# Optimization experiments

Hardware: AMD Instinct MI355X
Metric: run time of the kernel (lower is better)

The kernel has to match this reference:

```python
import jax, jax.numpy as jnp
import numpy as np

Q = 5
PAD = Q // 2
MAX_OFFSET = 5.0


def _conv3(x, w, b):
    # 3x3 SAME conv, NCHW / OIHW
    y = jax.lax.conv_general_dilated(x, w, (1, 1), 'SAME',
                                     dimension_numbers=('NCHW', 'OIHW', 'NCHW'))
    return y + b[None, :, None, None]


def _l2norm_c(x):
    # F.normalize(p=2, dim=1) with eps=1e-12
    n = jnp.sqrt(jnp.sum(x * x, axis=1, keepdims=True))
    return x / jnp.maximum(n, 1e-12)


def _cost_volume(Ha, Hb):
    # cost[b,k,h,w] = sum_c Ha[b,c,h,w] * Hb_pad[b,c,h+dy,w+dx], k = dy*Q+dx
    B, C, H, W = Ha.shape
    Ha = _l2norm_c(Ha)
    Hb = _l2norm_c(Hb)
    Hbp = jnp.pad(Hb, ((0, 0), (0, 0), (PAD, PAD), (PAD, PAD)))
    costs = [jnp.sum(Ha * jax.lax.dynamic_slice(Hbp, (0, 0, dy, dx), (B, C, H, W)), axis=1)
             for dy in range(Q) for dx in range(Q)]
    return jnp.stack(costs, axis=1)  # (B, Q*Q, H, W)


def _grid_sample_border(img, x, y):
    # bilinear, padding_mode='border', align_corners=True; x,y in pixel coords (B,H,W)
    B, C, H, W = img.shape
    x = jnp.clip(x, 0.0, W - 1.0)
    y = jnp.clip(y, 0.0, H - 1.0)
    x0 = jnp.floor(x)
    y0 = jnp.floor(y)
    x1 = jnp.minimum(x0 + 1.0, W - 1.0)
    y1 = jnp.minimum(y0 + 1.0, H - 1.0)
    wx = (x - x0)[:, None, :, :]
    wy = (y - y0)[:, None, :, :]
    x0i, x1i = x0.astype(jnp.int32), x1.astype(jnp.int32)
    y0i, y1i = y0.astype(jnp.int32), y1.astype(jnp.int32)
    imf = img.reshape(B, C, H * W)

    def gather(yi, xi):
        idx = (yi * W + xi).reshape(B, 1, H * W)
        return jnp.take_along_axis(imf, idx, axis=2).reshape(B, C, H, W)

    v00 = gather(y0i, x0i)
    v01 = gather(y0i, x1i)
    v10 = gather(y1i, x0i)
    v11 = gather(y1i, x1i)
    return (v00 * (1 - wx) * (1 - wy) + v01 * wx * (1 - wy)
            + v10 * (1 - wx) * wy + v11 * wx * wy)


def reference(pts_bev, img_bev, heatmap_pts, heatmap_img,
              fw1, fb1, fw2, fb2, gw1, gb1, gw2, gb2):
    B, C, H, W = pts_bev.shape
    dt = pts_bev.dtype
    # permute (0,1,3,2), detach, sigmoid
    hp = jax.nn.sigmoid(jax.lax.stop_gradient(jnp.transpose(heatmap_pts, (0, 1, 3, 2))))
    hi = jax.nn.sigmoid(jax.lax.stop_gradient(jnp.transpose(heatmap_img, (0, 1, 3, 2))))
    cp = _cost_volume(hp, hi)
    ci = _cost_volume(hi, hp)
    concat = jnp.concatenate([pts_bev, cp, img_bev, ci], axis=1)  # (B, 2C+2*Q^2, H, W)
    h = jax.nn.relu(_conv3(concat, fw1, fb1))
    flow = jnp.tanh(_conv3(h, fw2, fb2)) * MAX_OFFSET  # (B,4,H,W)
    base_x = jnp.arange(W, dtype=dt)[None, None, :]  # (1,1,W)
    base_y = jnp.arange(H, dtype=dt)[None, :, None]  # (1,H,1)
    src_px = base_x + flow[:, 0]
    src_py = base_y + flow[:, 1]
    src_ix = base_x + flow[:, 2]
    src_iy = base_y + flow[:, 3]
    aligned_p = _grid_sample_border(pts_bev, src_px, src_py)
    aligned_i = _grid_sample_border(img_bev, src_ix, src_iy)
    fused_in = jnp.concatenate([aligned_i, aligned_p], axis=1)
    fused = jax.nn.relu(_conv3(fused_in, gw1, gb1))
    fused = _conv3(fused, gw2, gb2)
    return fused


def setup_inputs() -> dict:
    key = jax.random.key(0)
    ks = jax.random.split(key, 12)
    B, C, H, W, NC = 4, 128, 180, 180, 10
    feat_in = 2 * C + 2 * Q * Q  # 306
    hid = 64
    s = 0.02
    return {
        'pts_bev': jax.random.normal(ks[0], (B, C, H, W), jnp.float32),
        'img_bev': jax.random.normal(ks[1], (B, C, H, W), jnp.float32),
        'heatmap_pts': jax.random.normal(ks[2], (B, NC, W, H), jnp.float32),
        'heatmap_img': jax.random.normal(ks[3], (B, NC, W, H), jnp.float32),
        'fw1': jax.random.normal(ks[4], (hid, feat_in, 3, 3), jnp.float32) * s,
        'fb1': jnp.zeros((hid,), jnp.float32),
        'fw2': jax.random.normal(ks[5], (4, hid, 3, 3), jnp.float32) * s,
        'fb2': jnp.zeros((4,), jnp.float32),
        'gw1': jax.random.normal(ks[6], (C, 2 * C, 3, 3), jnp.float32) * s,
        'gb1': jnp.zeros((C,), jnp.float32),
        'gw2': jax.random.normal(ks[7], (C, C, 3, 3), jnp.float32) * s,
        'gb2': jnp.zeros((C,), jnp.float32),
    }
```

## Files before the change

### kernel.cpp

```cpp
#include <hip/hip_runtime.h>
#include <cstdint>


constexpr int H = 180, W = 180, HW = H * W;
constexpr int PD = 194, PD2 = PD * PD;

typedef __attribute__((ext_vector_type(8))) short short8;
typedef __attribute__((ext_vector_type(4))) float f32x4;

constexpr size_t OFF_CAT  = 0;
constexpr size_t OFF_F2   = 0;
constexpr size_t R2       = 96348160;
constexpr size_t OFF_HPN  = R2;
constexpr size_t OFF_HIN  = R2 + 5184000;
constexpr size_t OFF_HBUF = R2;
constexpr size_t OFF_GO   = R2;
constexpr size_t R3       = R2 + 38539264;
constexpr size_t OFF_FLOW = R3;
constexpr size_t R4       = R3 + 2073600;
constexpr size_t OFF_WF1  = R4;
constexpr size_t OFF_WFG1 = R4 + 737280;
constexpr size_t OFF_WFG2 = R4 + 737280 + 1179648;

__device__ __forceinline__ unsigned short f2bf(float x) {
    unsigned int u = __builtin_bit_cast(unsigned int, x);
    unsigned int r = (u + 0x7FFFu + ((u >> 16) & 1u)) >> 16;
    return (unsigned short)r;
}
__device__ __forceinline__ float bf2f(unsigned short b) {
    return __builtin_bit_cast(float, (unsigned int)b << 16);
}

#define GLL(SRC, DST) __builtin_amdgcn_global_load_lds(                        \
    (const __attribute__((address_space(1))) unsigned int*)(SRC),              \
    (__attribute__((address_space(3))) unsigned int*)(DST), 16, 0, 0)

__global__ __launch_bounds__(256) void border_zero(unsigned short* __restrict__ buf,
                                                   int CPdiv8, int total) {
    int id = blockIdx.x * 256 + threadIdx.x;
    if (id >= total) return;
    int c8 = id % CPdiv8; int r = id / CPdiv8;
    int pi = r % 5236;    int b = r / 5236;
    int py, px;
    if (pi < 2716) { int ri = pi / 194; py = ri == 0 ? 0 : 180 + ri; px = pi % 194; }
    else { int j = pi - 2716; py = 1 + j / 14; int t = j % 14; px = t == 0 ? 0 : 180 + t; }
    short8 z = {0,0,0,0,0,0,0,0};
    *(short8*)&buf[((size_t)(b * PD + py) * PD + px) * (size_t)(CPdiv8 * 8) + c8 * 8] = z;
}

__global__ __launch_bounds__(192) void build_cat(const float* __restrict__ pts,
                                                 const float* __restrict__ img,
                                                 unsigned short* __restrict__ cat) {
    int b = blockIdx.x / 180, h = blockIdx.x % 180;
    int t = threadIdx.x;
    if (t >= 180) return;
    unsigned short* pb = cat + ((size_t)(b * PD + 1 + h) * PD + (1 + t)) * 320;
    const float* ps = pts + (size_t)b * 128 * HW + h * W + t;
    const float* is = img + (size_t)b * 128 * HW + h * W + t;
#pragma unroll 4
    for (int v = 0; v < 16; ++v) {
        short8 o;
#pragma unroll
        for (int e = 0; e < 8; ++e) o[e] = (short)f2bf(ps[(size_t)(v * 8 + e) * HW]);
        *(short8*)&pb[v * 8] = o;
    }
#pragma unroll 4
    for (int v = 0; v < 16; ++v) {
        short8 o;
#pragma unroll
        for (int e = 0; e < 8; ++e) o[e] = (short)f2bf(is[(size_t)(v * 8 + e) * HW]);
        *(short8*)&pb[128 + v * 8] = o;
    }
}

__global__ __launch_bounds__(256) void prep_heatmaps(
    const float* __restrict__ hm_pts, const float* __restrict__ hm_img,
    float* __restrict__ hpn, float* __restrict__ hin, int B) {
    __shared__ float s[10][16][17];
    const int t = threadIdx.x;
    const int tsel = blockIdx.z & 1, b = blockIdx.z >> 1;
    const int h0 = blockIdx.y * 16, w0 = blockIdx.x * 16;
    const float* src = tsel ? hm_img : hm_pts;
    float* dst = tsel ? hin : hpn;
    {
        const int th = t & 15, tw = t >> 4;
        const int gh = h0 + th, gw = w0 + tw;
        if (gh < H && gw < W) {
#pragma unroll
            for (int c = 0; c < 10; ++c)
                s[c][tw][th] = src[((size_t)(b * 10 + c) * W + gw) * H + gh];
        }
    }
    __syncthreads();
    const int wq = t & 15, hq = t >> 4;
    const int gh = h0 + hq, gw = w0 + wq;
    if (gh >= H || gw >= W) return;
    float v[10]; float ss = 0.f;
#pragma unroll
    for (int c = 0; c < 10; ++c) {
        float x = s[c][wq][hq];
        float sg = 1.f / (1.f + expf(-x));
        v[c] = sg; ss += sg * sg;
    }
    float inv = 1.f / fmaxf(sqrtf(ss), 1e-12f);
#pragma unroll
    for (int c = 0; c < 10; ++c)
        dst[(size_t)(b * 10 + c) * HW + gh * W + gw] = v[c] * inv;
}

__global__ __launch_bounds__(256) void cost_volume_cat(
    const float* __restrict__ hpn, const float* __restrict__ hin,
    unsigned short* __restrict__ cat, int B, int total) {
    int id = blockIdx.x * 256 + threadIdx.x;
    if (id >= total) return;
    int w = id % W; int r = id / W;
    int h = r % H;  int b = r / H;
    float hp_l[10], hi_l[10];
    size_t base = (size_t)b * 10 * HW + h * W + w;
#pragma unroll
    for (int c = 0; c < 10; ++c) {
        hp_l[c] = hpn[base + (size_t)c * HW];
        hi_l[c] = hin[base + (size_t)c * HW];
    }
    unsigned pk[32];
#pragma unroll
    for (int j = 0; j < 32; ++j) pk[j] = 0;
#pragma unroll
    for (int dy = 0; dy < 5; ++dy)
#pragma unroll
        for (int dx = 0; dx < 5; ++dx) {
            const int k = dy * 5 + dx;
            int yy = h + dy - 2, xx = w + dx - 2;
            float ap = 0.f, ai = 0.f;
            if (yy >= 0 && yy < H && xx >= 0 && xx < W) {
                size_t nb = (size_t)b * 10 * HW + yy * W + xx;
#pragma unroll
                for (int c = 0; c < 10; ++c) {
                    ap = fmaf(hp_l[c], hin[nb + (size_t)c * HW], ap);
                    ai = fmaf(hi_l[c], hpn[nb + (size_t)c * HW], ai);
                }
            }
            pk[k >> 1] |= (unsigned)f2bf(ap) << ((k & 1) * 16);
            const int kc = 25 + k;
            pk[kc >> 1] |= (unsigned)f2bf(ai) << ((kc & 1) * 16);
        }
    unsigned short* pb = cat + ((size_t)(b * PD + 1 + h) * PD + (1 + w)) * 320 + 256;
#pragma unroll
    for (int v = 0; v < 8; ++v) {
        uint4 q = {pk[v * 4], pk[v * 4 + 1], pk[v * 4 + 2], pk[v * 4 + 3]};
        *(uint4*)((char*)pb + v * 16) = q;
    }
}

template <int MODE>
__global__ __launch_bounds__(256) void wfrag_kernel(const float* __restrict__ w,
                                                    unsigned short* __restrict__ wf,
                                                    int Cin, int nOg, int nfrag) {
    int t = blockIdx.x * 256 + threadIdx.x;
    int f = t >> 6, lane = t & 63;
    if (f >= nfrag) return;
    int part = f & 1; int r = f >> 1;
    int og = r % nOg; r /= nOg;
    int tap = r % 9;  int chunk = r / 9;
    int oc = og * 16 + (lane & 15);
    short8 out;
#pragma unroll
    for (int e = 0; e < 8; ++e) {
        int c = chunk * 32 + ((lane >> 4) << 3) + e;
        int rc = c;
        if (MODE == 1) {
            if (c < 128) rc = c;
            else if (c < 256) rc = c + 25;
            else if (c < 281) rc = c - 128;
            else rc = c;
        }
        float val = 0.f;
        if (rc < Cin && (MODE == 0 || c < 306))
            val = w[((size_t)oc * Cin + rc) * 9 + tap];
        unsigned short hi = f2bf(val);
        out[e] = (short)(part == 0 ? hi : f2bf(val - bf2f(hi)));
    }
    *(short8*)&wf[(size_t)f * 512 + lane * 8] = out;
}

template <int NCH, int COUT, int EPI, bool RELU, int OCB>
__global__ __launch_bounds__(256, 2) void conv_mfma(
    const unsigned short* __restrict__ act,
    const unsigned short* __restrict__ wf,
    const float* __restrict__ bias,
    float* __restrict__ outF,
    unsigned short* __restrict__ outB,
    int Bn) {
    constexpr int CP = NCH * 32;
    constexpr int NOG = COUT / 16;
    constexpr int G = OCB / 16;
    __shared__ __align__(16) char ldsAll[2 * 20736 + 8192];

    const int tid = threadIdx.x;
    const int lane = tid & 63, wv = tid >> 6;
    const int zz = blockIdx.z;
    constexpr int NT = COUT / OCB;
    const int bb = zz / NT;
    const int oc0 = (zz % NT) * OCB;
    const int og0 = oc0 >> 4;
    const int y0 = blockIdx.y * 16, x0 = blockIdx.x * 16;

    const char* actB = (const char*)act + (size_t)bb * PD2 * CP * 2;

    unsigned soff[6];
#pragma unroll
    for (int i = 0; i < 6; ++i) {
        int idx = i * 256 + tid;
        int p = idx >> 2, q = idx & 3;
        int yy = p / 18, xx = p % 18;
        soff[i] = ((unsigned)((y0 + yy) * PD + (x0 + xx)) * CP + q * 8) * 2;
    }
    const int alane = (lane & 15) * 32 + ((lane >> 4) << 3);
    const unsigned short* wlane = wf + (size_t)og0 * 1024 + lane * 8;

    f32x4 acc[4][G];
#pragma unroll
    for (int i = 0; i < 4; ++i)
#pragma unroll
        for (int j = 0; j < G; ++j) acc[i][j] = (f32x4){0.f, 0.f, 0.f, 0.f};

    auto stage = [&](int chunk, int bsel) {
        unsigned co = (unsigned)chunk * 64;
#pragma unroll
        for (int i = 0; i < 5; ++i)
            GLL(actB + soff[i] + co,
                ldsAll + (size_t)bsel * 20736 + ((i << 8) + (wv << 6)) * 16);
        if (tid < 16)
            GLL(actB + soff[5] + co,
                ldsAll + (size_t)bsel * 20736 + ((5 << 8)) * 16);
    };
    auto loadW = [&](int idx, short8 (&dh)[G], short8 (&dl)[G]) {
        const unsigned short* p = wlane + (size_t)idx * NOG * 1024;
#pragma unroll
        for (int g = 0; g < G; ++g) {
            dh[g] = *(const short8*)(p + g * 1024);
            dl[g] = *(const short8*)(p + g * 1024 + 512);
        }
    };
    auto compTap = [&](int dy, int dx, const short8 (&bh)[G], const short8 (&bl)[G],
                       const unsigned short* tb) {
        __builtin_amdgcn_s_setprio(1);
#pragma unroll
        for (int rr = 0; rr < 4; ++rr) {
            const int yy = wv * 4 + rr + dy;
            short8 a = *(const short8*)(tb + (yy * 18 + dx) * 32 + alane);
#pragma unroll
            for (int g = 0; g < G; ++g) {
                asm("v_mfma_f32_16x16x32_bf16 %0, %1, %2, %0"
                    : "+v"(acc[rr][g]) : "v"(a), "v"(bh[g]));
                asm("v_mfma_f32_16x16x32_bf16 %0, %1, %2, %0"
                    : "+v"(acc[rr][g]) : "v"(a), "v"(bl[g]));
            }
        }
        __builtin_amdgcn_s_setprio(0);
    };

    short8 wh[2][G], wl[2][G];
    stage(0, 0);
    loadW(0, wh[0], wl[0]);
    asm volatile("s_waitcnt vmcnt(0)" ::: "memory");
    __syncthreads();

    int bsel = 0;
    for (int cp2 = 0; cp2 < NCH / 2; ++cp2) {
#pragma unroll
        for (int par = 0; par < 2; ++par) {
            const int chunk = cp2 * 2 + par;
            const unsigned short* tb = (const unsigned short*)ldsAll + bsel * 10368;
#pragma unroll
            for (int t = 0; t < 9; ++t) {
                const int cb = (t + par) & 1;
                if (t < 8) {
                    if (cb) loadW(chunk * 9 + t + 1, wh[0], wl[0]);
                    else    loadW(chunk * 9 + t + 1, wh[1], wl[1]);
                } else if (chunk + 1 < NCH) {
                    if (cb) loadW((chunk + 1) * 9, wh[0], wl[0]);
                    else    loadW((chunk + 1) * 9, wh[1], wl[1]);
                }
                if (t == 0 && chunk + 1 < NCH) stage(chunk + 1, bsel ^ 1);
                if (cb) compTap(t / 3, t % 3, wh[1], wl[1], tb);
                else    compTap(t / 3, t % 3, wh[0], wl[0], tb);
            }
            asm volatile("s_waitcnt vmcnt(0)" ::: "memory");
            __syncthreads();
            bsel ^= 1;
        }
    }

    float bv[G];
#pragma unroll
    for (int g = 0; g < G; ++g) bv[g] = bias[oc0 + g * 16 + (lane & 15)];

    if constexpr (EPI == 0) {
        float* sc = (float*)(ldsAll + 41472 + wv * 2048);
#pragma unroll
        for (int rr = 0; rr < 4; ++rr) {
            const int yy = y0 + wv * 4 + rr;
#pragma unroll
            for (int g = 0; g < G; ++g) {
                f32x4 v = acc[rr][g];
#pragma unroll
                for (int j = 0; j < 4; ++j) {
                    v[j] += bv[g];
                    if (RELU) v[j] = fmaxf(v[j], 0.f);
                }
                *(f32x4*)&sc[(lane & 15) * 20 + ((lane >> 4) << 2)] = v;
                asm volatile("s_waitcnt lgkmcnt(0)" ::: "memory");
                f32x4 rd = *(const f32x4*)&sc[(lane >> 2) * 20 + ((lane & 3) << 2)];
                const int oc = oc0 + g * 16 + (lane >> 2);
                const int xs = x0 + ((lane & 3) << 2);
                if (yy < H && xs < W)
                    *(f32x4*)&outF[((size_t)(bb * COUT + oc)) * HW + yy * W + xs] = rd;
                asm volatile("s_waitcnt lgkmcnt(0)" ::: "memory");
            }
        }
    } else {
        unsigned short* sb = (unsigned short*)(ldsAll + 41472 + wv * 2048);
#pragma unroll
        for (int rr = 0; rr < 4; ++rr) {
            const int yy = y0 + wv * 4 + rr;
#pragma unroll
            for (int g = 0; g < G; ++g)
#pragma unroll
                for (int r2 = 0; r2 < 4; ++r2) {
                    float v = acc[rr][g][r2] + bv[g];
                    if (RELU) v = fmaxf(v, 0.f);
                    sb[(((lane >> 4) << 2) + r2) * OCB + g * 16 + (lane & 15)] = f2bf(v);
                }
            asm volatile("s_waitcnt lgkmcnt(0)" ::: "memory");
#pragma unroll
            for (int j = 0; j < OCB / 32; ++j) {
                int idx = j * 64 + lane;
                int px = idx / (OCB / 8), c8 = idx % (OCB / 8);
                short8 rd = *(const short8*)&sb[px * OCB + c8 * 8];
                int gx = x0 + px;
                if (yy < H && gx < W)
                    *(short8*)&outB[((size_t)(bb * PD + 1 + yy) * PD + 1 + gx) * COUT
                                    + oc0 + c8 * 8] = rd;
            }
            asm volatile("s_waitcnt lgkmcnt(0)" ::: "memory");
        }
    }
}

__global__ __launch_bounds__(256) void conv_flow_kernel(
    const float* __restrict__ hbuf, const float* __restrict__ fw2,
    const float* __restrict__ fb2, float* __restrict__ flow, int B) {
    __shared__ __align__(16) float s_in[8][18][20];
    __shared__ __align__(16) float s_w[72][4];
    const int t = threadIdx.x;
    const int px = t & 15, py = t >> 4;
    const int b = blockIdx.z;
    const int ty0 = blockIdx.y * 16, tx0 = blockIdx.x * 16;
    float acc[4] = {0.f, 0.f, 0.f, 0.f};
    for (int chunk = 0; chunk < 8; ++chunk) {
        int c0 = chunk * 8;
        __syncthreads();
        for (int u = t; u < 8 * 18 * 18; u += 256) {
            int ch = u / 324, rem = u % 324;
            int row = rem / 18, col = rem % 18;
            int gy = ty0 + row - 1, gx = tx0 + col - 1;
            float v = 0.f;
            if (gy >= 0 && gy < H && gx >= 0 && gx < W)
                v = hbuf[(size_t)(b * 64 + c0 + ch) * HW + gy * W + gx];
            s_in[ch][row][col] = v;
        }
        for (int u = t; u < 288; u += 256) {
            int k = u >> 2, o = u & 3;
            int ch = k / 9, kk = k % 9;
            s_w[k][o] = fw2[(size_t)(o * 64 + c0 + ch) * 9 + kk];
        }
        __syncthreads();
#pragma unroll
        for (int ch = 0; ch < 8; ++ch)
#pragma unroll
            for (int ky = 0; ky < 3; ++ky)
#pragma unroll
                for (int kx = 0; kx < 3; ++kx) {
                    float a = s_in[ch][py + ky][px + kx];
                    const float4 w4 = *(const float4*)(&s_w[ch * 9 + ky * 3 + kx][0]);
                    acc[0] = fmaf(a, w4.x, acc[0]);
                    acc[1] = fmaf(a, w4.y, acc[1]);
                    acc[2] = fmaf(a, w4.z, acc[2]);
                    acc[3] = fmaf(a, w4.w, acc[3]);
                }
    }
    int y = ty0 + py, x = tx0 + px;
    if (y < H && x < W) {
#pragma unroll
        for (int o = 0; o < 4; ++o)
            flow[(size_t)(b * 4 + o) * HW + y * W + x] =
                tanhf(acc[o] + fb2[o]) * 5.0f;
    }
}

__global__ __launch_bounds__(256) void grid_sample_bf(
    const float* __restrict__ pts, const float* __restrict__ img,
    const float* __restrict__ flow, unsigned short* __restrict__ f2,
    int B, int total) {
    int id = blockIdx.x * 256 + threadIdx.x;
    if (id >= total) return;
    int w = id % W; int r = id / W;
    int h = r % H;  r /= H;
    int b = r % B;  int q = r / B;
    const bool is_img = q < 16;
    const int cb = (is_img ? q : q - 16) * 8;
    const float* src = is_img ? img : pts;
    const int fo = is_img ? 2 : 0;
    size_t fbase = (size_t)b * 4 * HW + h * W + w;
    float sx = (float)w + flow[fbase + (size_t)fo * HW];
    float sy = (float)h + flow[fbase + (size_t)(fo + 1) * HW];
    sx = fminf(fmaxf(sx, 0.f), (float)(W - 1));
    sy = fminf(fmaxf(sy, 0.f), (float)(H - 1));
    float x0f = floorf(sx), y0f = floorf(sy);
    float x1f = fminf(x0f + 1.f, (float)(W - 1));
    float y1f = fminf(y0f + 1.f, (float)(H - 1));
    float wx = sx - x0f, wy = sy - y0f;
    int x0 = (int)x0f, x1 = (int)x1f, y0 = (int)y0f, y1 = (int)y1f;
    float w00 = (1.f - wx) * (1.f - wy), w01 = wx * (1.f - wy);
    float w10 = (1.f - wx) * wy,         w11 = wx * wy;
    const float* sbp = src + (size_t)b * 128 * HW;
    short8 pack;
#pragma unroll
    for (int j = 0; j < 8; ++j) {
        const float* p = sbp + (size_t)(cb + j) * HW;
        float v = p[y0 * W + x0] * w00 + p[y0 * W + x1] * w01 +
                  p[y1 * W + x0] * w10 + p[y1 * W + x1] * w11;
        pack[j] = (short)f2bf(v);
    }
    *(short8*)&f2[((size_t)(b * PD + 1 + h) * PD + 1 + w) * 256 +
                  (is_img ? 0 : 128) + cb] = pack;
}

extern "C" void kernel_launch(void* const* d_in, const int* in_sizes, int n_in,
                              void* d_out, int out_size, void* d_ws, size_t ws_size,
                              hipStream_t stream) {
    const float* pts  = (const float*)d_in[0];
    const float* img  = (const float*)d_in[1];
    const float* hm_p = (const float*)d_in[2];
    const float* hm_i = (const float*)d_in[3];
    const float* fw1  = (const float*)d_in[4];
    const float* fb1  = (const float*)d_in[5];
    const float* fw2  = (const float*)d_in[6];
    const float* fb2  = (const float*)d_in[7];
    const float* gw1  = (const float*)d_in[8];
    const float* gb1  = (const float*)d_in[9];
    const float* gw2  = (const float*)d_in[10];
    const float* gb2  = (const float*)d_in[11];
    char* ws = (char*)d_ws;
    const int B = in_sizes[0] / (128 * HW);

    unsigned short* cat  = (unsigned short*)(ws + OFF_CAT);
    unsigned short* f2   = (unsigned short*)(ws + OFF_F2);
    unsigned short* go   = (unsigned short*)(ws + OFF_GO);
    float* hpn   = (float*)(ws + OFF_HPN);
    float* hin   = (float*)(ws + OFF_HIN);
    float* hbuf  = (float*)(ws + OFF_HBUF);
    float* flow  = (float*)(ws + OFF_FLOW);
    unsigned short* wf1  = (unsigned short*)(ws + OFF_WF1);
    unsigned short* wfg1 = (unsigned short*)(ws + OFF_WFG1);
    unsigned short* wfg2 = (unsigned short*)(ws + OFF_WFG2);

    wfrag_kernel<1><<<180, 256, 0, stream>>>(fw1, wf1, 306, 4, 720);
    wfrag_kernel<0><<<288, 256, 0, stream>>>(gw1, wfg1, 256, 8, 1152);
    wfrag_kernel<0><<<144, 256, 0, stream>>>(gw2, wfg2, 128, 8, 576);
    {
        int tot = B * 5236 * 40;
        border_zero<<<(tot + 255) / 256, 256, 0, stream>>>(cat, 40, tot);
    }
    build_cat<<<B * 180, 192, 0, stream>>>(pts, img, cat);
    {
        dim3 grid(12, 12, 2 * B);
        prep_heatmaps<<<grid, 256, 0, stream>>>(hm_p, hm_i, hpn, hin, B);
    }
    int totc = B * HW;
    cost_volume_cat<<<(totc + 255) / 256, 256, 0, stream>>>(hpn, hin, cat, B, totc);
    {
        dim3 grid(12, 12, 2 * B);
        conv_mfma<10, 64, 0, true, 32><<<grid, 256, 0, stream>>>(
            cat, wf1, fb1, hbuf, nullptr, B);
    }
    {
        dim3 grid(12, 12, B);
        conv_flow_kernel<<<grid, 256, 0, stream>>>(hbuf, fw2, fb2, flow, B);
    }
    {
        int tot = B * 5236 * 32;
        border_zero<<<(tot + 255) / 256, 256, 0, stream>>>(f2, 32, tot);
        int tot2 = B * 5236 * 16;
        border_zero<<<(tot2 + 255) / 256, 256, 0, stream>>>(go, 16, tot2);
    }
    int totg = 32 * B * HW;
    grid_sample_bf<<<(totg + 255) / 256, 256, 0, stream>>>(pts, img, flow, f2, B, totg);
    {
        dim3 grid(12, 12, 2 * B);
        conv_mfma<8, 128, 1, true, 64><<<grid, 256, 0, stream>>>(
            f2, wfg1, gb1, nullptr, go, B);
    }
    {
        dim3 grid(12, 12, 2 * B);
        conv_mfma<4, 128, 0, false, 64><<<grid, 256, 0, stream>>>(
            go, wfg2, gb2, (float*)d_out, nullptr, B);
    }
}
```

Baseline: 807.1 us.

## Switch intermediates to NHWC bf16 and sample from the padded concat buffer

Heatmap features are now stored pixel-major with 12 floats per pixel, so the cost volume reads each neighbour with three vector loads instead of ten strided ones. The first conv now writes its hidden activations as padded NHWC bf16. A new flow conv stages them into LDS with global_load_lds. Grid sampling now gathers 8-channel bf16 vectors from the already-built concat buffer instead of scalar fp32 loads from the raw inputs, and the workspace layout is reorganised so f2 no longer aliases cat. This cuts memory traffic and gathers, at the cost of extra bf16 rounding in the sampled features and flow inputs.

After: 2.874 ms. +256.1%, slower.

```diff
diff --git a/kernel.cpp b/kernel.cpp
--- a/kernel.cpp
+++ b/kernel.cpp
@@ -9,18 +9,17 @@
 typedef __attribute__((ext_vector_type(4))) float f32x4;
 
 constexpr size_t OFF_CAT  = 0;
-constexpr size_t OFF_F2   = 0;
-constexpr size_t R2       = 96348160;
+constexpr size_t OFF_F2   = 96348160;
+constexpr size_t R2       = OFF_F2 + 77078528;
 constexpr size_t OFF_HPN  = R2;
-constexpr size_t OFF_HIN  = R2 + 5184000;
+constexpr size_t OFF_HIN  = R2 + 6220800;
 constexpr size_t OFF_HBUF = R2;
-constexpr size_t OFF_GO   = R2;
-constexpr size_t R3       = R2 + 38539264;
-constexpr size_t OFF_FLOW = R3;
-constexpr size_t R4       = R3 + 2073600;
-constexpr size_t OFF_WF1  = R4;
-constexpr size_t OFF_WFG1 = R4 + 737280;
-constexpr size_t OFF_WFG2 = R4 + 737280 + 1179648;
+constexpr size_t R3       = R2 + 19269632;
+constexpr size_t OFF_GO   = R3;
+constexpr size_t OFF_FLOW = R3 + 38539264;
+constexpr size_t OFF_WF1  = OFF_FLOW + 2073600;
+constexpr size_t OFF_WFG1 = OFF_WF1 + 737280;
+constexpr size_t OFF_WFG2 = OFF_WFG1 + 1179648;
 
 __device__ __forceinline__ unsigned short f2bf(float x) {
     unsigned int u = __builtin_bit_cast(unsigned int, x);
@@ -103,9 +102,11 @@
         v[c] = sg; ss += sg * sg;
     }
     float inv = 1.f / fmaxf(sqrtf(ss), 1e-12f);
-#pragma unroll
-    for (int c = 0; c < 10; ++c)
-        dst[(size_t)(b * 10 + c) * HW + gh * W + gw] = v[c] * inv;
+    float* rec = dst + ((size_t)b * HW + gh * W + gw) * 12;
+    float4 q0 = {v[0] * inv, v[1] * inv, v[2] * inv, v[3] * inv};
+    float4 q1 = {v[4] * inv, v[5] * inv, v[6] * inv, v[7] * inv};
+    float4 q2 = {v[8] * inv, v[9] * inv, 0.f, 0.f};
+    *(float4*)rec = q0; *(float4*)(rec + 4) = q1; *(float4*)(rec + 8) = q2;
 }
 
 __global__ __launch_bounds__(256) void cost_volume_cat(
@@ -115,12 +116,22 @@
     if (id >= total) return;
     int w = id % W; int r = id / W;
     int h = r % H;  int b = r / H;
+    const float* hpb = hpn + (size_t)b * HW * 12;
+    const float* hib = hin + (size_t)b * HW * 12;
     float hp_l[10], hi_l[10];
-    size_t base = (size_t)b * 10 * HW + h * W + w;
-#pragma unroll
-    for (int c = 0; c < 10; ++c) {
-        hp_l[c] = hpn[base + (size_t)c * HW];
-        hi_l[c] = hin[base + (size_t)c * HW];
+    {
+        const float* c0 = hpb + (size_t)(h * W + w) * 12;
+        const float* c1 = hib + (size_t)(h * W + w) * 12;
+        float4 a0 = *(const float4*)c0, a1 = *(const float4*)(c0 + 4);
+        float4 a2 = *(const float4*)(c0 + 8);
+        float4 b0 = *(const float4*)c1, b1 = *(const float4*)(c1 + 4);
+        float4 b2 = *(const float4*)(c1 + 8);
+        hp_l[0]=a0.x; hp_l[1]=a0.y; hp_l[2]=a0.z; hp_l[3]=a0.w;
+        hp_l[4]=a1.x; hp_l[5]=a1.y; hp_l[6]=a1.z; hp_l[7]=a1.w;
+        hp_l[8]=a2.x; hp_l[9]=a2.y;
+        hi_l[0]=b0.x; hi_l[1]=b0.y; hi_l[2]=b0.z; hi_l[3]=b0.w;
+        hi_l[4]=b1.x; hi_l[5]=b1.y; hi_l[6]=b1.z; hi_l[7]=b1.w;
+        hi_l[8]=b2.x; hi_l[9]=b2.y;
     }
     unsigned pk[32];
 #pragma unroll
@@ -133,11 +144,25 @@
             int yy = h + dy - 2, xx = w + dx - 2;
             float ap = 0.f, ai = 0.f;
             if (yy >= 0 && yy < H && xx >= 0 && xx < W) {
-                size_t nb = (size_t)b * 10 * HW + yy * W + xx;
+                const float* n0 = hib + (size_t)(yy * W + xx) * 12;
+                const float* n1 = hpb + (size_t)(yy * W + xx) * 12;
+                float n0v[10], n1v[10];
+                {
+                    float4 u0=*(const float4*)n0, u1=*(const float4*)(n0+4);
+                    float4 u2=*(const float4*)(n0+8);
+                    float4 v0=*(const float4*)n1, v1=*(const float4*)(n1+4);
+                    float4 v2=*(const float4*)(n1+8);
+                    n0v[0]=u0.x;n0v[1]=u0.y;n0v[2]=u0.z;n0v[3]=u0.w;
+                    n0v[4]=u1.x;n0v[5]=u1.y;n0v[6]=u1.z;n0v[7]=u1.w;
+                    n0v[8]=u2.x;n0v[9]=u2.y;
+                    n1v[0]=v0.x;n1v[1]=v0.y;n1v[2]=v0.z;n1v[3]=v0.w;
+                    n1v[4]=v1.x;n1v[5]=v1.y;n1v[6]=v1.z;n1v[7]=v1.w;
+                    n1v[8]=v2.x;n1v[9]=v2.y;
+                }
 #pragma unroll
                 for (int c = 0; c < 10; ++c) {
-                    ap = fmaf(hp_l[c], hin[nb + (size_t)c * HW], ap);
-                    ai = fmaf(hi_l[c], hpn[nb + (size_t)c * HW], ai);
+                    ap = fmaf(hp_l[c], n0v[c], ap);
+                    ai = fmaf(hi_l[c], n1v[c], ai);
                 }
             }
             pk[k >> 1] |= (unsigned)f2bf(ap) << ((k & 1) * 16);
@@ -348,69 +373,79 @@
     }
 }
 
-__global__ __launch_bounds__(256) void conv_flow_kernel(
-    const float* __restrict__ hbuf, const float* __restrict__ fw2,
+__global__ __launch_bounds__(256) void conv_flow_nhwc(
+    const unsigned short* __restrict__ hbuf, const float* __restrict__ fw2,
     const float* __restrict__ fb2, float* __restrict__ flow, int B) {
-    __shared__ __align__(16) float s_in[8][18][20];
-    __shared__ __align__(16) float s_w[72][4];
+    __shared__ __align__(16) char lds[41472 + 9216];
+    unsigned short* s_in = (unsigned short*)lds;
+    float* s_w = (float*)(lds + 41472);
     const int t = threadIdx.x;
-    const int px = t & 15, py = t >> 4;
+    const int lane = t & 63, wv = t >> 6;
     const int b = blockIdx.z;
-    const int ty0 = blockIdx.y * 16, tx0 = blockIdx.x * 16;
-    float acc[4] = {0.f, 0.f, 0.f, 0.f};
-    for (int chunk = 0; chunk < 8; ++chunk) {
-        int c0 = chunk * 8;
-        __syncthreads();
-        for (int u = t; u < 8 * 18 * 18; u += 256) {
-            int ch = u / 324, rem = u % 324;
-            int row = rem / 18, col = rem % 18;
-            int gy = ty0 + row - 1, gx = tx0 + col - 1;
-            float v = 0.f;
-            if (gy >= 0 && gy < H && gx >= 0 && gx < W)
-                v = hbuf[(size_t)(b * 64 + c0 + ch) * HW + gy * W + gx];
-            s_in[ch][row][col] = v;
-        }
-        for (int u = t; u < 288; u += 256) {
-            int k = u >> 2, o = u & 3;
-            int ch = k / 9, kk = k % 9;
-            s_w[k][o] = fw2[(size_t)(o * 64 + c0 + ch) * 9 + kk];
-        }
-        __syncthreads();
-#pragma unroll
-        for (int ch = 0; ch < 8; ++ch)
-#pragma unroll
-            for (int ky = 0; ky < 3; ++ky)
-#pragma unroll
-                for (int kx = 0; kx < 3; ++kx) {
-                    float a = s_in[ch][py + ky][px + kx];
-                    const float4 w4 = *(const float4*)(&s_w[ch * 9 + ky * 3 + kx][0]);
+    const int y0 = blockIdx.y * 16, x0 = blockIdx.x * 16;
+    const char* base = (const char*)hbuf + ((size_t)(b * PD + y0) * PD + x0) * 128;
+#pragma unroll
+    for (int g = 0; g < 10; ++g) {
+        int idx = (wv * 10 + g) * 64 + lane;
+        int c8 = idx / 324, rem = idx % 324;
+        int row = rem / 18, col = rem % 18;
+        GLL(base + ((size_t)row * PD + col) * 128 + c8 * 16,
+            lds + (wv * 10 + g) * 1024);
+    }
+    if (wv == 3 && lane < 32) {
+        int idx = 2560 + lane;
+        int c8 = idx / 324, rem = idx % 324;
+        int row = rem / 18, col = rem % 18;
+        GLL(base + ((size_t)row * PD + col) * 128 + c8 * 16, lds + 40960);
+    }
+#pragma unroll
+    for (int i = 0; i < 9; ++i) {
+        int u = i * 256 + t;
+        int o = u & 3, tap = (u >> 2) % 9, ch = u / 36;
+        s_w[(ch * 9 + tap) * 4 + o] = fw2[(size_t)(o * 64 + ch) * 9 + tap];
+    }
+    asm volatile("s_waitcnt vmcnt(0)" ::: "memory");
+    __syncthreads();
+
+    const int py = t >> 4, px = t & 15;
+    float acc[4] = {fb2[0], fb2[1], fb2[2], fb2[3]};
+#pragma unroll
+    for (int c8 = 0; c8 < 8; ++c8)
+#pragma unroll
+        for (int ky = 0; ky < 3; ++ky)
+#pragma unroll
+            for (int kx = 0; kx < 3; ++kx) {
+                short8 a8 = *(const short8*)&s_in[(((c8 * 18) + py + ky) * 18
+                                                  + px + kx) * 8];
+                const float* wp = &s_w[(c8 * 8 * 9 + (ky * 3 + kx)) * 4];
+#pragma unroll
+                for (int e = 0; e < 8; ++e) {
+                    float a = bf2f((unsigned short)a8[e]);
+                    float4 w4 = *(const float4*)(wp + e * 36);
                     acc[0] = fmaf(a, w4.x, acc[0]);
                     acc[1] = fmaf(a, w4.y, acc[1]);
                     acc[2] = fmaf(a, w4.z, acc[2]);
                     acc[3] = fmaf(a, w4.w, acc[3]);
                 }
-    }
-    int y = ty0 + py, x = tx0 + px;
-    if (y < H && x < W) {
+            }
+    int h = y0 + py, w = x0 + px;
+    if (h < H && w < W) {
 #pragma unroll
         for (int o = 0; o < 4; ++o)
-            flow[(size_t)(b * 4 + o) * HW + y * W + x] =
-                tanhf(acc[o] + fb2[o]) * 5.0f;
-    }
-}
-
-__global__ __launch_bounds__(256) void grid_sample_bf(
-    const float* __restrict__ pts, const float* __restrict__ img,
-    const float* __restrict__ flow, unsigned short* __restrict__ f2,
-    int B, int total) {
+            flow[(size_t)(b * 4 + o) * HW + h * W + w] = tanhf(acc[o]) * 5.0f;
+    }
+}
+
+__global__ __launch_bounds__(256) void grid_sample_cat(
+    const unsigned short* __restrict__ cat, const float* __restrict__ flow,
+    unsigned short* __restrict__ f2, int B, int total) {
     int id = blockIdx.x * 256 + threadIdx.x;
     if (id >= total) return;
-    int w = id % W; int r = id / W;
-    int h = r % H;  r /= H;
-    int b = r % B;  int q = r / B;
+    int q = id & 31; int pix = id >> 5;
+    int w = pix % W; int r = pix / W;
+    int h = r % H;  int b = r / H;
     const bool is_img = q < 16;
-    const int cb = (is_img ? q : q - 16) * 8;
-    const float* src = is_img ? img : pts;
+    const int j = is_img ? q : q - 16;
     const int fo = is_img ? 2 : 0;
     size_t fbase = (size_t)b * 4 * HW + h * W + w;
     float sx = (float)w + flow[fbase + (size_t)fo * HW];
@@ -424,17 +459,23 @@
     int x0 = (int)x0f, x1 = (int)x1f, y0 = (int)y0f, y1 = (int)y1f;
     float w00 = (1.f - wx) * (1.f - wy), w01 = wx * (1.f - wy);
     float w10 = (1.f - wx) * wy,         w11 = wx * wy;
-    const float* sbp = src + (size_t)b * 128 * HW;
+    const unsigned short* cb0 = cat + (size_t)b * PD2 * 320
+                                + (is_img ? 128 : 0) + j * 8;
+    const short8 v00 = *(const short8*)&cb0[((size_t)(1 + y0) * PD + 1 + x0) * 320];
+    const short8 v01 = *(const short8*)&cb0[((size_t)(1 + y0) * PD + 1 + x1) * 320];
+    const short8 v10 = *(const short8*)&cb0[((size_t)(1 + y1) * PD + 1 + x0) * 320];
+    const short8 v11 = *(const short8*)&cb0[((size_t)(1 + y1) * PD + 1 + x1) * 320];
     short8 pack;
 #pragma unroll
-    for (int j = 0; j < 8; ++j) {
-        const float* p = sbp + (size_t)(cb + j) * HW;
-        float v = p[y0 * W + x0] * w00 + p[y0 * W + x1] * w01 +
-                  p[y1 * W + x0] * w10 + p[y1 * W + x1] * w11;
-        pack[j] = (short)f2bf(v);
+    for (int e = 0; e < 8; ++e) {
+        float v = bf2f((unsigned short)v00[e]) * w00 +
+                  bf2f((unsigned short)v01[e]) * w01 +
+                  bf2f((unsigned short)v10[e]) * w10 +
+                  bf2f((unsigned short)v11[e]) * w11;
+        pack[e] = (short)f2bf(v);
     }
     *(short8*)&f2[((size_t)(b * PD + 1 + h) * PD + 1 + w) * 256 +
-                  (is_img ? 0 : 128) + cb] = pack;
+                  (is_img ? 0 : 128) + j * 8] = pack;
 }
 
 extern "C" void kernel_launch(void* const* d_in, const int* in_sizes, int n_in,
@@ -457,10 +498,10 @@
 
     unsigned short* cat  = (unsigned short*)(ws + OFF_CAT);
     unsigned short* f2   = (unsigned short*)(ws + OFF_F2);
+    unsigned short* hbuf = (unsigned short*)(ws + OFF_HBUF);
     unsigned short* go   = (unsigned short*)(ws + OFF_GO);
     float* hpn   = (float*)(ws + OFF_HPN);
     float* hin   = (float*)(ws + OFF_HIN);
-    float* hbuf  = (float*)(ws + OFF_HBUF);
     float* flow  = (float*)(ws + OFF_FLOW);
     unsigned short* wf1  = (unsigned short*)(ws + OFF_WF1);
     unsigned short* wfg1 = (unsigned short*)(ws + OFF_WFG1);
@@ -481,13 +522,15 @@
     int totc = B * HW;
     cost_volume_cat<<<(totc + 255) / 256, 256, 0, stream>>>(hpn, hin, cat, B, totc);
     {
+        int tot = B * 5236 * 8;
+        border_zero<<<(tot + 255) / 256, 256, 0, stream>>>(hbuf, 8, tot);
         dim3 grid(12, 12, 2 * B);
-        conv_mfma<10, 64, 0, true, 32><<<grid, 256, 0, stream>>>(
-            cat, wf1, fb1, hbuf, nullptr, B);
+        conv_mfma<10, 64, 1, true, 32><<<grid, 256, 0, stream>>>(
+            cat, wf1, fb1, nullptr, hbuf, B);
     }
     {
         dim3 grid(12, 12, B);
-        conv_flow_kernel<<<grid, 256, 0, stream>>>(hbuf, fw2, fb2, flow, B);
+        conv_flow_nhwc<<<grid, 256, 0, stream>>>(hbuf, fw2, fb2, flow, B);
     }
     {
         int tot = B * 5236 * 32;
@@ -495,8 +538,8 @@
         int tot2 = B * 5236 * 16;
         border_zero<<<(tot2 + 255) / 256, 256, 0, stream>>>(go, 16, tot2);
     }
-    int totg = 32 * B * HW;
-    grid_sample_bf<<<(totg + 255) / 256, 256, 0, stream>>>(pts, img, flow, f2, B, totg);
+    int totg = B * HW * 32;
+    grid_sample_cat<<<(totg + 255) / 256, 256, 0, stream>>>(cat, flow, f2, B, totg);
     {
         dim3 grid(12, 12, 2 * B);
         conv_mfma<8, 128, 1, true, 64><<<grid, 256, 0, stream>>>(
```
